# Performance work log

Hardware: AMD Instinct MI355X
Metric: run time of the kernel (lower is better)

Reference implementation:

```python
import jax, jax.numpy as jnp
import numpy as np

ENC_DIM, DEC_DIM, ATT_DIM = 2048, 512, 512


def setup_inputs() -> dict:
    key = jax.random.key(0)
    ks = jax.random.split(key, 8)
    s = lambda d: 1.0 / np.sqrt(d)
    return {
        "encoder_features": jax.random.normal(ks[0], (256, ENC_DIM, 14, 14), jnp.float32),
        "decoder_hidden": jax.random.normal(ks[1], (256, DEC_DIM), jnp.float32),
        "W_enc": jax.random.uniform(ks[2], (ENC_DIM, ATT_DIM), jnp.float32, -s(ENC_DIM), s(ENC_DIM)),
        "b_enc": jax.random.uniform(ks[3], (ATT_DIM,), jnp.float32, -s(ENC_DIM), s(ENC_DIM)),
        "W_dec": jax.random.uniform(ks[4], (DEC_DIM, ATT_DIM), jnp.float32, -s(DEC_DIM), s(DEC_DIM)),
        "b_dec": jax.random.uniform(ks[5], (ATT_DIM,), jnp.float32, -s(DEC_DIM), s(DEC_DIM)),
        "W_full": jax.random.uniform(ks[6], (ATT_DIM, 1), jnp.float32, -s(ATT_DIM), s(ATT_DIM)),
        "b_full": jax.random.uniform(ks[7], (1,), jnp.float32, -s(ATT_DIM), s(ATT_DIM)),
    }


def reference(encoder_features, decoder_hidden, W_enc, b_enc, W_dec, b_dec, W_full, b_full):
    B, C, H, W = encoder_features.shape
    # [B, P, C] with P = H*W pixels
    feats = encoder_features.reshape(B, C, H * W).transpose(0, 2, 1)
    enc_att = jnp.einsum('bpc,ca->bpa', feats, W_enc) + b_enc            # [B,P,A]
    dec_att = decoder_hidden @ W_dec + b_dec                              # [B,A]
    att = jnp.einsum('bpa,a->bp', jax.nn.relu(enc_att + dec_att[:, None, :]), W_full[:, 0]) + b_full[0]
    alpha = jax.nn.softmax(att, axis=1)                                   # [B,P]
    context = jnp.einsum('bpc,bp->bc', feats, alpha)                      # [B,C]
    return (context, alpha)
```

## Files before the change

### kernel.cpp

```cpp
#include <hip/hip_runtime.h>

typedef unsigned short u16;
typedef __bf16 bf16x8 __attribute__((ext_vector_type(8)));
typedef float f32x4 __attribute__((ext_vector_type(4)));

#define B_   256
#define C_   2048
#define P_   196
#define A_   512
#define CP_  (C_ * P_)
#define MTOT (B_ * P_)

#define BM 64
#define BK 32
#define NBLK (MTOT / BM)

__device__ __forceinline__ u16 f2bf(float f) {
    unsigned int x = __float_as_uint(f);
    unsigned int r = (x + 0x7fffu + ((x >> 16) & 1u)) >> 16;
    return (u16)r;
}

__device__ __forceinline__ unsigned long long pack4bf(const float* v) {
    unsigned int lo = (unsigned int)f2bf(v[0]) | ((unsigned int)f2bf(v[1]) << 16);
    unsigned int hi = (unsigned int)f2bf(v[2]) | ((unsigned int)f2bf(v[3]) << 16);
    return (unsigned long long)lo | ((unsigned long long)hi << 32);
}

#define WG_BARRIER() asm volatile("s_waitcnt lgkmcnt(0)\n\ts_barrier" ::: "memory")

__global__ __launch_bounds__(256) void k_transpose_wenc(const float* __restrict__ W,
                                                        u16* __restrict__ Wt) {
    __shared__ u16 tile[64][65];
    int t  = threadIdx.x;
    int cb = (blockIdx.x & 31) * 64;
    int ab = (blockIdx.x >> 5) * 64;
#pragma unroll
    for (int i = 0; i < 16; ++i) {
        int c = (t >> 6) + i * 4;
        int a = t & 63;
        tile[c][a] = f2bf(W[(size_t)(cb + c) * A_ + ab + a]);
    }
    __syncthreads();
#pragma unroll
    for (int i = 0; i < 16; ++i) {
        int a  = (t >> 6) + i * 4;
        int cl = t & 63;
        Wt[(size_t)(ab + a) * C_ + cb + cl] = tile[cl][a];
    }
}

__global__ __launch_bounds__(512) void k_dec_att(const float* __restrict__ dh,
                                                 const float* __restrict__ Wd,
                                                 const float* __restrict__ bd,
                                                 float* __restrict__ out) {
    __shared__ float hL[512];
    int b = blockIdx.x, t = threadIdx.x;
    hL[t] = dh[b * 512 + t];
    __syncthreads();
    float s = bd[t];
#pragma unroll 8
    for (int k = 0; k < 512; ++k) s = fmaf(hL[k], Wd[k * 512 + t], s);
    out[b * 512 + t] = s;
}

__global__ __launch_bounds__(512, 4) void k_gemm_att(const float* __restrict__ enc,
                                                     const u16* __restrict__ Wt,
                                                     const float* __restrict__ dec_att,
                                                     const float* __restrict__ benc,
                                                     const float* __restrict__ wfull,
                                                     const float* __restrict__ bfull,
                                                     float* __restrict__ att) {
    __shared__ u16   As[2][4 * 512];
    __shared__ float decL[2][512];
    __shared__ float wL[512];
    __shared__ float att_part[8][64];

    const int t    = threadIdx.x;
    const int lane = t & 63;
    const int wa   = t >> 6;
    const int l16  = lane & 15;
    const int lq   = lane >> 4;
    const int row0 = blockIdx.x * BM;

    const int b0 = row0 / 196;
    const int b1 = (row0 + BM - 1) / 196;
    decL[0][t] = dec_att[b0 * 512 + t] + benc[t];
    decL[1][t] = dec_att[b1 * 512 + t] + benc[t];
    wL[t] = wfull[t];

    const int kq = t & 7;
    const int pl = t >> 3;
    const int pg = row0 + pl;
    const int bb = pg / 196;
    const int pp = pg - bb * 196;
    const float* srcA = enc + (size_t)bb * CP_ + (size_t)(kq * 4) * P_ + pp;
    const int a_off = (pl >> 4) * 512 + ((pl & 15) + 16 * (kq >> 1)) * 8 + (kq & 1) * 4;

    const u16* srcB = Wt + (size_t)(wa * 64 + l16) * C_ + lq * 8;

    f32x4 acc[4][4] = {};

    float av0[4], av1[4];
#pragma unroll
    for (int j = 0; j < 4; ++j) av0[j] = srcA[(size_t)j * P_];
    *(unsigned long long*)&As[0][a_off] = pack4bf(av0);
#pragma unroll
    for (int j = 0; j < 4; ++j) av1[j] = srcA[(size_t)BK * P_ + (size_t)j * P_];
    bf16x8 bcur[4];
#pragma unroll
    for (int ta = 0; ta < 4; ++ta)
        bcur[ta] = *(const bf16x8*)(srcB + (size_t)(ta * 16) * C_);
    WG_BARRIER();

    for (int k = 0; k < C_ / BK; k += 2) {
        bf16x8 bfr[4];
#pragma unroll
        for (int tr = 0; tr < 4; ++tr)
            bfr[tr] = *(const bf16x8*)&As[0][tr * 512 + lane * 8];
        if (k + 2 < C_ / BK) {
#pragma unroll
            for (int j = 0; j < 4; ++j)
                av0[j] = srcA[(size_t)(k + 2) * BK * P_ + (size_t)j * P_];
        }
#pragma unroll
        for (int ta = 0; ta < 4; ++ta)
#pragma unroll
            for (int tr = 0; tr < 4; ++tr)
                acc[ta][tr] = __builtin_amdgcn_mfma_f32_16x16x32_bf16(bcur[ta], bfr[tr],
                                                                      acc[ta][tr], 0, 0, 0);
#pragma unroll
        for (int ta = 0; ta < 4; ++ta)
            bcur[ta] = *(const bf16x8*)(srcB + (size_t)(ta * 16) * C_ + (size_t)(k + 1) * 32);
        *(unsigned long long*)&As[1][a_off] = pack4bf(av1);
        WG_BARRIER();

#pragma unroll
        for (int tr = 0; tr < 4; ++tr)
            bfr[tr] = *(const bf16x8*)&As[1][tr * 512 + lane * 8];
        if (k + 3 < C_ / BK) {
#pragma unroll
            for (int j = 0; j < 4; ++j)
                av1[j] = srcA[(size_t)(k + 3) * BK * P_ + (size_t)j * P_];
        }
#pragma unroll
        for (int ta = 0; ta < 4; ++ta)
#pragma unroll
            for (int tr = 0; tr < 4; ++tr)
                acc[ta][tr] = __builtin_amdgcn_mfma_f32_16x16x32_bf16(bcur[ta], bfr[tr],
                                                                      acc[ta][tr], 0, 0, 0);
        if (k + 2 < C_ / BK) {
#pragma unroll
            for (int ta = 0; ta < 4; ++ta)
                bcur[ta] = *(const bf16x8*)(srcB + (size_t)(ta * 16) * C_ + (size_t)(k + 2) * 32);
            *(unsigned long long*)&As[0][a_off] = pack4bf(av0);
        }
        WG_BARRIER();
    }

    const int col = l16, quad = lq;
#pragma unroll
    for (int tr = 0; tr < 4; ++tr) {
        int rgl = tr * 16 + col;
        int bi  = (row0 + rgl) / 196 - b0;
        float s = 0.0f;
#pragma unroll
        for (int ta = 0; ta < 4; ++ta)
#pragma unroll
            for (int rr = 0; rr < 4; ++rr) {
                int a_idx = wa * 64 + ta * 16 + quad * 4 + rr;
                float v = acc[ta][tr][rr] + decL[bi][a_idx];
                s = fmaf(fmaxf(v, 0.0f), wL[a_idx], s);
            }
        s += __shfl_xor(s, 16);
        s += __shfl_xor(s, 32);
        if (quad == 0) att_part[wa][rgl] = s;
    }
    __syncthreads();
    if (t < BM) {
        float s = bfull[0];
#pragma unroll
        for (int w = 0; w < 8; ++w) s += att_part[w][t];
        att[row0 + t] = s;
    }
}

__global__ __launch_bounds__(64) void k_softmax(const float* __restrict__ att,
                                                float* __restrict__ alpha) {
    int b = blockIdx.x, lane = threadIdx.x;
    const float* a = att + b * P_;
    float v[4];
    float mx = -__builtin_inff();
#pragma unroll
    for (int i = 0; i < 4; ++i) {
        int p = lane + i * 64;
        v[i] = (p < P_) ? a[p] : -__builtin_inff();
        mx = fmaxf(mx, v[i]);
    }
#pragma unroll
    for (int off = 32; off >= 1; off >>= 1) mx = fmaxf(mx, __shfl_xor(mx, off));
    float sum = 0.0f;
#pragma unroll
    for (int i = 0; i < 4; ++i) {
        int p = lane + i * 64;
        float e = (p < P_) ? expf(v[i] - mx) : 0.0f;
        v[i] = e;
        sum += e;
    }
#pragma unroll
    for (int off = 32; off >= 1; off >>= 1) sum += __shfl_xor(sum, off);
    float inv = 1.0f / sum;
#pragma unroll
    for (int i = 0; i < 4; ++i) {
        int p = lane + i * 64;
        if (p < P_) alpha[b * P_ + p] = v[i] * inv;
    }
}

__global__ __launch_bounds__(256) void k_context(const float* __restrict__ enc,
                                                 const float* __restrict__ alpha,
                                                 float* __restrict__ ctx) {
    __shared__ float aL[200];
    int t = threadIdx.x;
    int b = blockIdx.x >> 5;
    int chunk = blockIdx.x & 31;
    if (t < P_) aL[t] = alpha[b * P_ + t];
    __syncthreads();
    int wv = t >> 6, l = t & 63, g = l >> 4, j = l & 15;
    float4 a0 = *(const float4*)&aL[j * 4];
    float4 a1 = *(const float4*)&aL[64 + j * 4];
    float4 a2 = *(const float4*)&aL[128 + j * 4];
    float4 a3 = *(const float4*)&aL[192];
    const float* base = enc + (size_t)b * CP_ + (size_t)(chunk * 64) * P_;
#pragma unroll
    for (int pass = 0; pass < 4; ++pass) {
        int r = wv * 16 + pass * 4 + g;
        const float* row = base + (size_t)r * P_;
        float4 f0 = *(const float4*)(row + j * 4);
        float4 f1 = *(const float4*)(row + 64 + j * 4);
        float4 f2 = *(const float4*)(row + 128 + j * 4);
        float s = f0.x * a0.x + f0.y * a0.y + f0.z * a0.z + f0.w * a0.w;
        s += f1.x * a1.x + f1.y * a1.y + f1.z * a1.z + f1.w * a1.w;
        s += f2.x * a2.x + f2.y * a2.y + f2.z * a2.z + f2.w * a2.w;
        if (j == 0) {
            float4 f3 = *(const float4*)(row + 192);
            s += f3.x * a3.x + f3.y * a3.y + f3.z * a3.z + f3.w * a3.w;
        }
        s += __shfl_xor(s, 1);
        s += __shfl_xor(s, 2);
        s += __shfl_xor(s, 4);
        s += __shfl_xor(s, 8);
        if (j == 0) ctx[(size_t)b * C_ + chunk * 64 + r] = s;
    }
}

extern "C" void kernel_launch(void* const* d_in, const int* in_sizes, int n_in,
                              void* d_out, int out_size, void* d_ws, size_t ws_size,
                              hipStream_t stream) {
    const float* enc   = (const float*)d_in[0];
    const float* dh    = (const float*)d_in[1];
    const float* Wenc  = (const float*)d_in[2];
    const float* benc  = (const float*)d_in[3];
    const float* Wdec  = (const float*)d_in[4];
    const float* bdec  = (const float*)d_in[5];
    const float* wfull = (const float*)d_in[6];
    const float* bfull = (const float*)d_in[7];

    u16*   Wt  = (u16*)d_ws;
    float* dec = (float*)((char*)d_ws + (2u << 20));
    float* att = (float*)((char*)d_ws + (2u << 20) + (512u << 10));

    float* ctx     = (float*)d_out;
    float* alpha_o = ctx + B_ * C_;

    k_transpose_wenc<<<dim3(256), dim3(256), 0, stream>>>(Wenc, Wt);
    k_dec_att<<<dim3(256), dim3(512), 0, stream>>>(dh, Wdec, bdec, dec);
    k_gemm_att<<<dim3(NBLK), dim3(512), 0, stream>>>(enc, Wt, dec, benc,
                                                     wfull, bfull, att);
    k_softmax<<<dim3(256), dim3(64), 0, stream>>>(att, alpha_o);
    k_context<<<dim3(256 * 32), dim3(256), 0, stream>>>(enc, alpha_o, ctx);
}
```

Before: 905.9 us.

## Stream W_enc tiles into LDS asynchronously and deepen A-operand prefetch pipeline

The attention GEMM now brings W_enc tiles straight into a double-buffered LDS region with global_load_lds, instead of loading them into registers. The main loop is rewritten as an unrolled macro with an explicit vmcnt-based barrier, so outstanding global loads can stay in flight across iterations. Encoder-feature prefetch is extended to three register stages, and the epilogue scratch reuses the A buffer. The new 64KB B buffer sharply raises LDS use per block, which likely cuts resident blocks per CU below the launch-bounds target of 4.

```diff
diff --git a/kernel.cpp b/kernel.cpp
--- a/kernel.cpp
+++ b/kernel.cpp
@@ -27,7 +27,14 @@
     return (unsigned long long)lo | ((unsigned long long)hi << 32);
 }
 
-#define WG_BARRIER() asm volatile("s_waitcnt lgkmcnt(0)\n\ts_barrier" ::: "memory")
+__device__ __forceinline__ void gl_lds16(const void* g, void* l) {
+    __builtin_amdgcn_global_load_lds(
+        (const __attribute__((address_space(1))) unsigned int*)g,
+        (__attribute__((address_space(3))) unsigned int*)l, 16, 0, 0);
+}
+
+#define FENCE() asm volatile("" ::: "memory")
+#define BAR_VM(N) asm volatile("s_waitcnt vmcnt(" #N ") lgkmcnt(0)\n\ts_barrier" ::: "memory")
 
 __global__ __launch_bounds__(256) void k_transpose_wenc(const float* __restrict__ W,
                                                         u16* __restrict__ Wt) {
@@ -63,6 +70,39 @@
     for (int k = 0; k < 512; ++k) s = fmaf(hL[k], Wd[k * 512 + t], s);
     out[b * 512 + t] = s;
 }
+
+#define GEMM_BODY(KK, P, AV, DO_B, DO_PACK, DO_A, VMN)                               \
+  {                                                                                  \
+    if (DO_B) {                                                                      \
+      const u16* sB = srcB + (size_t)((KK) + 1) * 32;                                \
+      gl_lds16(sB,                   &Bs[(P) ^ 1][b_off]);                           \
+      gl_lds16(sB + (size_t)16 * C_, &Bs[(P) ^ 1][b_off + 512]);                     \
+      gl_lds16(sB + (size_t)32 * C_, &Bs[(P) ^ 1][b_off + 1024]);                    \
+      gl_lds16(sB + (size_t)48 * C_, &Bs[(P) ^ 1][b_off + 1536]);                    \
+      FENCE();                                                                       \
+    }                                                                                \
+    bf16x8 bfr[4];                                                                   \
+    _Pragma("unroll")                                                                \
+    for (int tr = 0; tr < 4; ++tr)                                                   \
+      bfr[tr] = *(const bf16x8*)&As[P][tr * 512 + lane * 8];                         \
+    _Pragma("unroll")                                                                \
+    for (int ta = 0; ta < 4; ++ta) {                                                 \
+      bf16x8 afr = *(const bf16x8*)&Bs[P][(wv * 4 + ta) * 512 + lane * 8];           \
+      _Pragma("unroll")                                                              \
+      for (int tr = 0; tr < 4; ++tr)                                                 \
+        acc[ta][tr] = __builtin_amdgcn_mfma_f32_16x16x32_bf16(afr, bfr[tr],          \
+                                                              acc[ta][tr], 0, 0, 0); \
+    }                                                                                \
+    if (DO_PACK)                                                                     \
+      *(unsigned long long*)&As[(P) ^ 1][a_off] = pack4bf(AV);                       \
+    if (DO_A) {                                                                      \
+      const float* sA = srcA + (size_t)((KK) + 3) * BK * P_;                         \
+      _Pragma("unroll")                                                              \
+      for (int j = 0; j < 4; ++j) AV[j] = sA[j * P_];                                \
+      FENCE();                                                                       \
+    }                                                                                \
+    BAR_VM(VMN);                                                                     \
+  }
 
 __global__ __launch_bounds__(512, 4) void k_gemm_att(const float* __restrict__ enc,
                                                      const u16* __restrict__ Wt,
@@ -72,13 +112,14 @@
                                                      const float* __restrict__ bfull,
                                                      float* __restrict__ att) {
     __shared__ u16   As[2][4 * 512];
+    __shared__ u16   Bs[2][32 * 512];
     __shared__ float decL[2][512];
     __shared__ float wL[512];
-    __shared__ float att_part[8][64];
+    float* att_part = (float*)&As[0][0];
 
     const int t    = threadIdx.x;
     const int lane = t & 63;
-    const int wa   = t >> 6;
+    const int wv   = t >> 6;
     const int l16  = lane & 15;
     const int lq   = lane >> 4;
     const int row0 = blockIdx.x * BM;
@@ -97,66 +138,36 @@
     const float* srcA = enc + (size_t)bb * CP_ + (size_t)(kq * 4) * P_ + pp;
     const int a_off = (pl >> 4) * 512 + ((pl & 15) + 16 * (kq >> 1)) * 8 + (kq & 1) * 4;
 
-    const u16* srcB = Wt + (size_t)(wa * 64 + l16) * C_ + lq * 8;
+    const u16* srcB  = Wt + (size_t)(wv * 64 + l16) * C_ + lq * 8;
+    const int  b_off = (wv * 4) * 512 + lane * 8;
 
     f32x4 acc[4][4] = {};
 
-    float av0[4], av1[4];
-#pragma unroll
-    for (int j = 0; j < 4; ++j) av0[j] = srcA[(size_t)j * P_];
-    *(unsigned long long*)&As[0][a_off] = pack4bf(av0);
-#pragma unroll
-    for (int j = 0; j < 4; ++j) av1[j] = srcA[(size_t)BK * P_ + (size_t)j * P_];
-    bf16x8 bcur[4];
-#pragma unroll
-    for (int ta = 0; ta < 4; ++ta)
-        bcur[ta] = *(const bf16x8*)(srcB + (size_t)(ta * 16) * C_);
-    WG_BARRIER();
-
-    for (int k = 0; k < C_ / BK; k += 2) {
-        bf16x8 bfr[4];
-#pragma unroll
-        for (int tr = 0; tr < 4; ++tr)
-            bfr[tr] = *(const bf16x8*)&As[0][tr * 512 + lane * 8];
-        if (k + 2 < C_ / BK) {
-#pragma unroll
-            for (int j = 0; j < 4; ++j)
-                av0[j] = srcA[(size_t)(k + 2) * BK * P_ + (size_t)j * P_];
-        }
-#pragma unroll
-        for (int ta = 0; ta < 4; ++ta)
-#pragma unroll
-            for (int tr = 0; tr < 4; ++tr)
-                acc[ta][tr] = __builtin_amdgcn_mfma_f32_16x16x32_bf16(bcur[ta], bfr[tr],
-                                                                      acc[ta][tr], 0, 0, 0);
-#pragma unroll
-        for (int ta = 0; ta < 4; ++ta)
-            bcur[ta] = *(const bf16x8*)(srcB + (size_t)(ta * 16) * C_ + (size_t)(k + 1) * 32);
-        *(unsigned long long*)&As[1][a_off] = pack4bf(av1);
-        WG_BARRIER();
-
-#pragma unroll
-        for (int tr = 0; tr < 4; ++tr)
-            bfr[tr] = *(const bf16x8*)&As[1][tr * 512 + lane * 8];
-        if (k + 3 < C_ / BK) {
-#pragma unroll
-            for (int j = 0; j < 4; ++j)
-                av1[j] = srcA[(size_t)(k + 3) * BK * P_ + (size_t)j * P_];
-        }
-#pragma unroll
-        for (int ta = 0; ta < 4; ++ta)
-#pragma unroll
-            for (int tr = 0; tr < 4; ++tr)
-                acc[ta][tr] = __builtin_amdgcn_mfma_f32_16x16x32_bf16(bcur[ta], bfr[tr],
-                                                                      acc[ta][tr], 0, 0, 0);
-        if (k + 2 < C_ / BK) {
-#pragma unroll
-            for (int ta = 0; ta < 4; ++ta)
-                bcur[ta] = *(const bf16x8*)(srcB + (size_t)(ta * 16) * C_ + (size_t)(k + 2) * 32);
-            *(unsigned long long*)&As[0][a_off] = pack4bf(av0);
-        }
-        WG_BARRIER();
-    }
+    float avT[4], av0[4], av1[4];
+#pragma unroll
+    for (int j = 0; j < 4; ++j) avT[j] = srcA[(size_t)j * P_];
+    gl_lds16(srcB,                   &Bs[0][b_off]);
+    gl_lds16(srcB + (size_t)16 * C_, &Bs[0][b_off + 512]);
+    gl_lds16(srcB + (size_t)32 * C_, &Bs[0][b_off + 1024]);
+    gl_lds16(srcB + (size_t)48 * C_, &Bs[0][b_off + 1536]);
+    FENCE();
+#pragma unroll
+    for (int j = 0; j < 4; ++j) av1[j] = srcA[(size_t)1 * BK * P_ + j * P_];
+#pragma unroll
+    for (int j = 0; j < 4; ++j) av0[j] = srcA[(size_t)2 * BK * P_ + j * P_];
+    FENCE();
+    *(unsigned long long*)&As[0][a_off] = pack4bf(avT);
+    BAR_VM(8);
+
+#pragma unroll 1
+    for (int k = 0; k < 60; k += 2) {
+        GEMM_BODY(k,     0, av1, 1, 1, 1, 4);
+        GEMM_BODY(k + 1, 1, av0, 1, 1, 1, 4);
+    }
+    GEMM_BODY(60, 0, av1, 1, 1, 1, 4);
+    GEMM_BODY(61, 1, av0, 1, 1, 0, 0);
+    GEMM_BODY(62, 0, av1, 1, 1, 0, 0);
+    GEMM_BODY(63, 1, av0, 0, 0, 0, 0);
 
     const int col = l16, quad = lq;
 #pragma unroll
@@ -168,19 +179,19 @@
         for (int ta = 0; ta < 4; ++ta)
 #pragma unroll
             for (int rr = 0; rr < 4; ++rr) {
-                int a_idx = wa * 64 + ta * 16 + quad * 4 + rr;
+                int a_idx = wv * 64 + ta * 16 + quad * 4 + rr;
                 float v = acc[ta][tr][rr] + decL[bi][a_idx];
                 s = fmaf(fmaxf(v, 0.0f), wL[a_idx], s);
             }
         s += __shfl_xor(s, 16);
         s += __shfl_xor(s, 32);
-        if (quad == 0) att_part[wa][rgl] = s;
+        if (quad == 0) att_part[wv * 64 + rgl] = s;
     }
     __syncthreads();
     if (t < BM) {
         float s = bfull[0];
 #pragma unroll
-        for (int w = 0; w < 8; ++w) s += att_part[w][t];
+        for (int w = 0; w < 8; ++w) s += att_part[w * 64 + t];
         att[row0 + t] = s;
     }
 }
```

Result: no change. 920.3 us (+1.6%).
